# Performance work log

Measured on AMD Instinct MI355X. Metric: run time of the kernel, lower is better.

## Reference

```python
import jax, jax.numpy as jnp
import numpy as np

FS = 4096.0
TRAIN_KERNEL = 4
TRAIN_STRIDE = 0.25
BATCH = 1024
NPERSEG = 4096          # fftlength * fs
NOVERLAP = NPERSEG // 2 # default overlap
FL, FH = 20.0, 500.0


def _welch(data):
    """Faithful port of _torch_welch with average='mean' (which is a SUM over segments
    in the original code), off by the same constant factor as the original."""
    N, nsample = data.shape
    nstride = NPERSEG - NOVERLAP
    nseg = int(np.ceil((nsample - NPERSEG) / nstride)) + 1
    # frame indices [nseg, nperseg] (static numpy -> cheap gather)
    idx = np.arange(nseg)[:, None] * nstride + np.arange(NPERSEG)[None, :]
    frames = data[:, idx]                                   # [N, nseg, nperseg]
    n = np.arange(NPERSEG)
    window = (0.5 - 0.5 * np.cos(2.0 * np.pi * n / NPERSEG)).astype(np.float32) * 2.0  # periodic hann * 2
    fd = jnp.fft.rfft(frames * window, axis=-1)             # [N, nseg, nfreq]
    power = jnp.real(fd) ** 2 + jnp.imag(fd) ** 2
    psd = jnp.sum(power, axis=1)                            # original 'mean' branch uses sum
    T = nsample * FS
    return psd / T                                          # [N, nfreq]


def setup_inputs() -> dict:
    key = jax.random.key(0)
    k1, k2 = jax.random.split(key)
    T = int(TRAIN_KERNEL * FS)  # 16384
    pred = jax.random.normal(k1, (BATCH, T), dtype=jnp.float32)
    target = jax.random.normal(k2, (BATCH, T), dtype=jnp.float32)
    return {"pred": pred, "target": target}


def reference(pred, target):
    res = target - pred
    s = int(TRAIN_STRIDE * FS)                     # 1024 samples per stride
    shape_x = int(TRAIN_KERNEL / TRAIN_STRIDE)     # 16
    # cross[i] = res[:, i*s:(i+1)*s].flatten() -> reshape/transpose, no loop
    def to_cross(x):
        return x[:, : shape_x * s].reshape(BATCH, shape_x, s).transpose(1, 0, 2).reshape(shape_x, BATCH * s)
    cross_res = to_cross(res)
    cross_target = to_cross(target)

    psd_res = _welch(cross_res)                    # [shape_x, nfreq]
    psd_target = _welch(cross_target)

    nfreq = NPERSEG // 2 + 1
    freq = np.linspace(0.0, FS / 2.0, nfreq)
    mask = jnp.asarray((FL < freq) & (freq < FH))
    dfreq = float(freq[1] - freq[0])
    scale = FH - FL

    psd_res = jnp.where(mask, psd_res, 0.0)
    psd_ratio = psd_res / psd_target
    loss = jnp.sum(psd_ratio, axis=1) * dfreq / scale  # [shape_x]
    return jnp.mean(loss[-8:]) * loss.shape[0]
```

## Files before the change

### kernel.cpp

```cpp
#include <hip/hip_runtime.h>

#define NSEG 511
#define NROWS 8
#define ROW0 8
#define K0 21
#define KEND 500
#define NFREQ 479
#define ACC_STRIDE 512
#define ACC_ELEMS (2 * NROWS * ACC_STRIDE)
#define NREP 8
#define NBLOCKS (2 * NROWS * NSEG)

__device__ __forceinline__ int sw(int i) { return i ^ (((i >> 5) & 7) << 2); }

__device__ __forceinline__ int dr_pos(int k) {
    return ((k >> 9) & 3) + 4 * ((k >> 6) & 7) + 32 * ((k >> 3) & 7) + 256 * (k & 7);
}

__device__ __forceinline__ float2 cmul(float2 a, float2 b) {
    return make_float2(fmaf(a.x, b.x, -a.y * b.y), fmaf(a.x, b.y, a.y * b.x));
}
__device__ __forceinline__ float2 cadd(float2 a, float2 b) { return make_float2(a.x + b.x, a.y + b.y); }
__device__ __forceinline__ float2 csub(float2 a, float2 b) { return make_float2(a.x - b.x, a.y - b.y); }

__device__ __forceinline__ void dft8(float2& x0, float2& x1, float2& x2, float2& x3,
                                     float2& x4, float2& x5, float2& x6, float2& x7) {
    const float C45 = 0.70710678118654752440f;
    float2 t0 = cadd(x0, x4), u0 = csub(x0, x4);
    float2 t1 = cadd(x1, x5), u1 = csub(x1, x5);
    float2 t2 = cadd(x2, x6), u2 = csub(x2, x6);
    float2 t3 = cadd(x3, x7), u3 = csub(x3, x7);
    float2 s0 = cadd(t0, t2), d0 = csub(t0, t2);
    float2 s1 = cadd(t1, t3), d1 = csub(t1, t3);
    float2 v1 = make_float2(C45 * (u1.x + u1.y), C45 * (u1.y - u1.x));
    float2 v2 = make_float2(u2.y, -u2.x);
    float2 v3 = make_float2(C45 * (u3.y - u3.x), -C45 * (u3.x + u3.y));
    float2 s2 = cadd(u0, v2), d2 = csub(u0, v2);
    float2 s3 = cadd(v1, v3), d3 = csub(v1, v3);
    float2 mid1 = make_float2(d1.y, -d1.x);
    float2 mid3 = make_float2(d3.y, -d3.x);
    x0 = cadd(s0, s1); x4 = csub(s0, s1);
    x2 = cadd(d0, mid1); x6 = csub(d0, mid1);
    x1 = cadd(s2, s3); x5 = csub(s2, s3);
    x3 = cadd(d2, mid3); x7 = csub(d2, mid3);
}

__device__ __forceinline__ void twiddle8(float2& x1, float2& x2, float2& x3, float2& x4,
                                         float2& x5, float2& x6, float2& x7, float ang) {
    float s, c;
    __sincosf(ang, &s, &c);
    float2 w1 = make_float2(c, s);
    float2 w2 = cmul(w1, w1);
    float2 w3 = cmul(w2, w1);
    float2 w4 = cmul(w2, w2);
    float2 w5 = cmul(w4, w1);
    float2 w6 = cmul(w3, w3);
    float2 w7 = cmul(w4, w3);
    x1 = cmul(x1, w1); x2 = cmul(x2, w2); x3 = cmul(x3, w3);
    x4 = cmul(x4, w4); x5 = cmul(x5, w5); x6 = cmul(x6, w6);
    x7 = cmul(x7, w7);
}

__global__ __launch_bounds__(256)
void psd_kernel(const float* __restrict__ pred,
                const float* __restrict__ target,
                float* __restrict__ acc) {
    __shared__ float2 buf[2048];

    const int bid = blockIdx.x;
    const int seg = bid % NSEG;
    const int row = (bid / NSEG) % NROWS + ROW0;
    const int sig = bid / (NSEG * NROWS);
    const int tid = threadIdx.x;
    float* accR = acc + (bid & (NREP - 1)) * ACC_ELEMS;

    const float2* t2p = (const float2*)target;
    const float2* p2p = (const float2*)pred;

    const float WA = 3.06796157577128245e-3f;
    const float CD = 0.99999882344642529f;
    const float SD = 1.53398018628476550e-3f;
    const int base2 = 2 * seg * 8192 + row * 512 + tid;
    float2 x0, x1, x2, x3, x4, x5, x6, x7;
#define LOADW(R, X)                                                          \
    {                                                                        \
        int idx2 = base2 + ((R) >> 1) * 8192 + ((R) & 1) * 256;              \
        float2 v = t2p[idx2];                                                \
        if (sig == 0) { float2 p = p2p[idx2]; v.x -= p.x; v.y -= p.y; }      \
        float sa, ca;                                                        \
        __sincosf((float)(tid + 256 * (R)) * WA, &sa, &ca);                  \
        X = make_float2(v.x * (1.0f - ca),                                   \
                        v.y * (1.0f - (ca * CD - sa * SD)));                 \
    }
    LOADW(0, x0) LOADW(1, x1) LOADW(2, x2) LOADW(3, x3)
    LOADW(4, x4) LOADW(5, x5) LOADW(6, x6) LOADW(7, x7)
#undef LOADW

    dft8(x0, x1, x2, x3, x4, x5, x6, x7);
    twiddle8(x1, x2, x3, x4, x5, x6, x7, (float)tid * -3.06796157577128245e-3f);
    buf[sw(tid)]        = x0;
    buf[sw(tid + 256)]  = x1;
    buf[sw(tid + 512)]  = x2;
    buf[sw(tid + 768)]  = x3;
    buf[sw(tid + 1024)] = x4;
    buf[sw(tid + 1280)] = x5;
    buf[sw(tid + 1536)] = x6;
    buf[sw(tid + 1792)] = x7;
    __syncthreads();

    {
        const int pb = tid >> 5, q0 = tid & 31;
        const int baseB = q0 + 256 * pb;
        x0 = buf[sw(baseB)];
        x1 = buf[sw(baseB + 32)];
        x2 = buf[sw(baseB + 64)];
        x3 = buf[sw(baseB + 96)];
        x4 = buf[sw(baseB + 128)];
        x5 = buf[sw(baseB + 160)];
        x6 = buf[sw(baseB + 192)];
        x7 = buf[sw(baseB + 224)];
        dft8(x0, x1, x2, x3, x4, x5, x6, x7);
        twiddle8(x1, x2, x3, x4, x5, x6, x7, (float)q0 * -2.45436926061702596e-2f);
        buf[sw(baseB)]       = x0;
        buf[sw(baseB + 32)]  = x1;
        buf[sw(baseB + 64)]  = x2;
        buf[sw(baseB + 96)]  = x3;
        buf[sw(baseB + 128)] = x4;
        buf[sw(baseB + 160)] = x5;
        buf[sw(baseB + 192)] = x6;
        buf[sw(baseB + 224)] = x7;
    }
    __syncthreads();

    {
        const int pb2 = tid >> 5, j2 = (tid >> 2) & 7, mq = tid & 3;
        const int baseC = mq + 32 * j2 + 256 * pb2;
        x0 = buf[sw(baseC)];
        x1 = buf[sw(baseC + 4)];
        x2 = buf[sw(baseC + 8)];
        x3 = buf[sw(baseC + 12)];
        x4 = buf[sw(baseC + 16)];
        x5 = buf[sw(baseC + 20)];
        x6 = buf[sw(baseC + 24)];
        x7 = buf[sw(baseC + 28)];
        dft8(x0, x1, x2, x3, x4, x5, x6, x7);
        twiddle8(x1, x2, x3, x4, x5, x6, x7, (float)mq * -1.96349540849362077e-1f);
        buf[sw(baseC)]      = x0;
        buf[sw(baseC + 4)]  = x1;
        buf[sw(baseC + 8)]  = x2;
        buf[sw(baseC + 12)] = x3;
        buf[sw(baseC + 16)] = x4;
        buf[sw(baseC + 20)] = x5;
        buf[sw(baseC + 24)] = x6;
        buf[sw(baseC + 28)] = x7;
    }
    __syncthreads();

    float4* b4 = (float4*)buf;
#define STAGE_D(G)                                                           \
    {                                                                        \
        int pbase = sw(4 * (tid + 256 * (G)));                               \
        float4 lo = b4[(pbase >> 1)];                                        \
        float4 hi = b4[(pbase >> 1) + 1];                                    \
        float2 a0 = make_float2(lo.x, lo.y), a1 = make_float2(lo.z, lo.w);   \
        float2 a2 = make_float2(hi.x, hi.y), a3 = make_float2(hi.z, hi.w);   \
        float2 S0 = cadd(a0, a2), D0 = csub(a0, a2);                         \
        float2 S1 = cadd(a1, a3), D1 = csub(a1, a3);                         \
        float2 mi = make_float2(D1.y, -D1.x);                                \
        float2 X0 = cadd(S0, S1), X2 = csub(S0, S1);                         \
        float2 X1 = cadd(D0, mi), X3 = csub(D0, mi);                         \
        b4[(pbase >> 1)]     = make_float4(X0.x, X0.y, X1.x, X1.y);          \
        b4[(pbase >> 1) + 1] = make_float4(X2.x, X2.y, X3.x, X3.y);          \
    }
    STAGE_D(0) STAGE_D(1)
#undef STAGE_D
    __syncthreads();

#define UNTANGLE(RR)                                                         \
    {                                                                        \
        int k = K0 + tid + 256 * (RR);                                       \
        if (k < KEND) {                                                      \
            float2 zk = buf[sw(dr_pos(k))];                                  \
            float2 zn = buf[sw(dr_pos(2048 - k))];                           \
            float Ex = 0.5f * (zk.x + zn.x);                                 \
            float Ey = 0.5f * (zk.y - zn.y);                                 \
            float Ox = 0.5f * (zk.y + zn.y);                                 \
            float Oy = -0.5f * (zk.x - zn.x);                                \
            float sn, cs;                                                    \
            __sincosf(-1.53398078788564123e-3f * (float)k, &sn, &cs);        \
            float xr = Ex + Ox * cs - Oy * sn;                               \
            float xi = Ey + Ox * sn + Oy * cs;                               \
            float pw = xr * xr + xi * xi;                                    \
            atomicAdd(&accR[(sig * NROWS + (row - ROW0)) * ACC_STRIDE + (k - K0)], pw); \
        }                                                                    \
    }
    UNTANGLE(0) UNTANGLE(1)
#undef UNTANGLE
}

__global__ __launch_bounds__(256)
void reduce_kernel(const float* __restrict__ acc, float* __restrict__ out) {
    __shared__ float sh[256];
    int tid = threadIdx.x;
    float sum = 0.0f;
    for (int n = tid; n < NROWS * NFREQ; n += 256) {
        int r = n / NFREQ, k = n % NFREQ;
        float num = 0.0f, den = 0.0f;
        #pragma unroll
        for (int rep = 0; rep < NREP; ++rep) {
            num += acc[rep * ACC_ELEMS + r * ACC_STRIDE + k];
            den += acc[rep * ACC_ELEMS + (NROWS + r) * ACC_STRIDE + k];
        }
        sum += num / den;
    }
    sh[tid] = sum;
    __syncthreads();
    for (int s = 128; s > 0; s >>= 1) {
        if (tid < s) sh[tid] += sh[tid + s];
        __syncthreads();
    }
    if (tid == 0) out[0] = sh[0] * (1.0f / 240.0f);
}

extern "C" void kernel_launch(void* const* d_in, const int* in_sizes, int n_in,
                              void* d_out, int out_size, void* d_ws, size_t ws_size,
                              hipStream_t stream) {
    const float* pred = (const float*)d_in[0];
    const float* target = (const float*)d_in[1];
    float* acc = (float*)d_ws;

    hipMemsetAsync(acc, 0, NREP * ACC_ELEMS * sizeof(float), stream);
    psd_kernel<<<NBLOCKS, 256, 0, stream>>>(pred, target, acc);
    reduce_kernel<<<1, 256, 0, stream>>>(acc, (float*)d_out);
}
```

Before: 190.3 us.

## Fuse final radix-4 stage into untangle and cut sincos and barrier costs

The last radix-4 FFT stage is folded into the real-FFT untangle step. Each output bin now reads its four partial values straight from shared memory and combines them in registers, which removes one shared-memory pass and one block barrier. Per-element sincos calls are replaced with symmetry rotations of a single sincos, a small constant table and an incremental rotation for the second bin. One __syncthreads is swapped for an s_waitcnt, which is only safe because each wavefront writes and then reads only its own data. The k-to-thread mapping also changes, which alters the shared-memory access pattern and the atomic addresses, and rotation-based twiddles may differ slightly in precision.

```diff
diff --git a/kernel.cpp b/kernel.cpp
--- a/kernel.cpp
+++ b/kernel.cpp
@@ -12,10 +12,6 @@
 #define NBLOCKS (2 * NROWS * NSEG)
 
 __device__ __forceinline__ int sw(int i) { return i ^ (((i >> 5) & 7) << 2); }
-
-__device__ __forceinline__ int dr_pos(int k) {
-    return ((k >> 9) & 3) + 4 * ((k >> 6) & 7) + 32 * ((k >> 3) & 7) + 256 * (k & 7);
-}
 
 __device__ __forceinline__ float2 cmul(float2 a, float2 b) {
     return make_float2(fmaf(a.x, b.x, -a.y * b.y), fmaf(a.x, b.y, a.y * b.x));
@@ -45,10 +41,9 @@
     x3 = cadd(d2, mid3); x7 = csub(d2, mid3);
 }
 
-__device__ __forceinline__ void twiddle8(float2& x1, float2& x2, float2& x3, float2& x4,
-                                         float2& x5, float2& x6, float2& x7, float ang) {
-    float s, c;
-    __sincosf(ang, &s, &c);
+__device__ __forceinline__ void twiddle8cs(float2& x1, float2& x2, float2& x3, float2& x4,
+                                           float2& x5, float2& x6, float2& x7,
+                                           float c, float s) {
     float2 w1 = make_float2(c, s);
     float2 w2 = cmul(w1, w1);
     float2 w3 = cmul(w2, w1);
@@ -80,24 +75,33 @@
     const float WA = 3.06796157577128245e-3f;
     const float CD = 0.99999882344642529f;
     const float SD = 1.53398018628476550e-3f;
+    const float H  = 0.70710678118654752440f;
+    float sa, ca;
+    __sincosf((float)tid * WA, &sa, &ca);
+
     const int base2 = 2 * seg * 8192 + row * 512 + tid;
     float2 x0, x1, x2, x3, x4, x5, x6, x7;
-#define LOADW(R, X)                                                          \
+#define LOADW(R, X, CE, SE)                                                  \
     {                                                                        \
         int idx2 = base2 + ((R) >> 1) * 8192 + ((R) & 1) * 256;              \
         float2 v = t2p[idx2];                                                \
         if (sig == 0) { float2 p = p2p[idx2]; v.x -= p.x; v.y -= p.y; }      \
-        float sa, ca;                                                        \
-        __sincosf((float)(tid + 256 * (R)) * WA, &sa, &ca);                  \
-        X = make_float2(v.x * (1.0f - ca),                                   \
-                        v.y * (1.0f - (ca * CD - sa * SD)));                 \
-    }
-    LOADW(0, x0) LOADW(1, x1) LOADW(2, x2) LOADW(3, x3)
-    LOADW(4, x4) LOADW(5, x5) LOADW(6, x6) LOADW(7, x7)
+        float cr = (CE), sr = (SE);                                          \
+        X = make_float2(v.x * (1.0f - cr),                                   \
+                        v.y * (1.0f - (cr * CD - sr * SD)));                 \
+    }
+    LOADW(0, x0, ca, sa)
+    LOADW(1, x1, H * (ca - sa), H * (sa + ca))
+    LOADW(2, x2, -sa, ca)
+    LOADW(3, x3, -H * (ca + sa), H * (ca - sa))
+    LOADW(4, x4, -ca, -sa)
+    LOADW(5, x5, H * (sa - ca), -H * (sa + ca))
+    LOADW(6, x6, sa, -ca)
+    LOADW(7, x7, H * (ca + sa), H * (sa - ca))
 #undef LOADW
 
     dft8(x0, x1, x2, x3, x4, x5, x6, x7);
-    twiddle8(x1, x2, x3, x4, x5, x6, x7, (float)tid * -3.06796157577128245e-3f);
+    twiddle8cs(x1, x2, x3, x4, x5, x6, x7, ca, -sa);
     buf[sw(tid)]        = x0;
     buf[sw(tid + 256)]  = x1;
     buf[sw(tid + 512)]  = x2;
@@ -120,7 +124,9 @@
         x6 = buf[sw(baseB + 192)];
         x7 = buf[sw(baseB + 224)];
         dft8(x0, x1, x2, x3, x4, x5, x6, x7);
-        twiddle8(x1, x2, x3, x4, x5, x6, x7, (float)q0 * -2.45436926061702596e-2f);
+        float sb, cb;
+        __sincosf((float)q0 * -2.45436926061702596e-2f, &sb, &cb);
+        twiddle8cs(x1, x2, x3, x4, x5, x6, x7, cb, sb);
         buf[sw(baseB)]       = x0;
         buf[sw(baseB + 32)]  = x1;
         buf[sw(baseB + 64)]  = x2;
@@ -130,7 +136,7 @@
         buf[sw(baseB + 192)] = x6;
         buf[sw(baseB + 224)] = x7;
     }
-    __syncthreads();
+    asm volatile("s_waitcnt lgkmcnt(0)" ::: "memory");
 
     {
         const int pb2 = tid >> 5, j2 = (tid >> 2) & 7, mq = tid & 3;
@@ -144,7 +150,12 @@
         x6 = buf[sw(baseC + 24)];
         x7 = buf[sw(baseC + 28)];
         dft8(x0, x1, x2, x3, x4, x5, x6, x7);
-        twiddle8(x1, x2, x3, x4, x5, x6, x7, (float)mq * -1.96349540849362077e-1f);
+        const float TC1 = 0.98078528040323044913f, TS1 = -0.19509032201612826785f;
+        const float TC2 = 0.92387953251128675613f, TS2 = -0.38268343236508977173f;
+        const float TC3 = 0.83146961230254523708f, TS3 = -0.55557023301960222474f;
+        float cc = (mq & 2) ? ((mq & 1) ? TC3 : TC2) : ((mq & 1) ? TC1 : 1.0f);
+        float ss = (mq & 2) ? ((mq & 1) ? TS3 : TS2) : ((mq & 1) ? TS1 : 0.0f);
+        twiddle8cs(x1, x2, x3, x4, x5, x6, x7, cc, ss);
         buf[sw(baseC)]      = x0;
         buf[sw(baseC + 4)]  = x1;
         buf[sw(baseC + 8)]  = x2;
@@ -156,45 +167,44 @@
     }
     __syncthreads();
 
-    float4* b4 = (float4*)buf;
-#define STAGE_D(G)                                                           \
+    const int kk0 = K0 + (((tid & 7) << 6) | (tid >> 3));
+    float sn0, cs0;
+    __sincosf(-1.53398078788564123e-3f * (float)kk0, &sn0, &cs0);
+#define UNTANGLE(KK, CS, SN)                                                 \
     {                                                                        \
-        int pbase = sw(4 * (tid + 256 * (G)));                               \
-        float4 lo = b4[(pbase >> 1)];                                        \
-        float4 hi = b4[(pbase >> 1) + 1];                                    \
-        float2 a0 = make_float2(lo.x, lo.y), a1 = make_float2(lo.z, lo.w);   \
-        float2 a2 = make_float2(hi.x, hi.y), a3 = make_float2(hi.z, hi.w);   \
-        float2 S0 = cadd(a0, a2), D0 = csub(a0, a2);                         \
-        float2 S1 = cadd(a1, a3), D1 = csub(a1, a3);                         \
-        float2 mi = make_float2(D1.y, -D1.x);                                \
-        float2 X0 = cadd(S0, S1), X2 = csub(S0, S1);                         \
-        float2 X1 = cadd(D0, mi), X3 = csub(D0, mi);                         \
-        b4[(pbase >> 1)]     = make_float4(X0.x, X0.y, X1.x, X1.y);          \
-        b4[(pbase >> 1) + 1] = make_float4(X2.x, X2.y, X3.x, X3.y);          \
-    }
-    STAGE_D(0) STAGE_D(1)
-#undef STAGE_D
-    __syncthreads();
-
-#define UNTANGLE(RR)                                                         \
-    {                                                                        \
-        int k = K0 + tid + 256 * (RR);                                       \
-        if (k < KEND) {                                                      \
-            float2 zk = buf[sw(dr_pos(k))];                                  \
-            float2 zn = buf[sw(dr_pos(2048 - k))];                           \
+        int kk = (KK);                                                       \
+        if (kk < KEND) {                                                     \
+            int bk = 4 * ((kk >> 6) & 7) + 32 * ((kk >> 3) & 7) + 256 * (kk & 7); \
+            int sbk = sw(bk);                                                \
+            float2 a0 = buf[sbk], a1 = buf[sbk + 1];                         \
+            float2 a2 = buf[sbk + 2], a3 = buf[sbk + 3];                     \
+            float2 zk = make_float2((a0.x + a2.x) + (a1.x + a3.x),           \
+                                    (a0.y + a2.y) + (a1.y + a3.y));          \
+            int m = 2048 - kk;                                               \
+            int bm = 4 * ((m >> 6) & 7) + 32 * ((m >> 3) & 7) + 256 * (m & 7); \
+            int sbm = sw(bm);                                                \
+            float2 b0 = buf[sbm], b1 = buf[sbm + 1];                         \
+            float2 b2 = buf[sbm + 2], b3 = buf[sbm + 3];                     \
+            float2 zn = make_float2((b0.x - b2.x) - (b1.y - b3.y),           \
+                                    (b0.y - b2.y) + (b1.x - b3.x));          \
             float Ex = 0.5f * (zk.x + zn.x);                                 \
             float Ey = 0.5f * (zk.y - zn.y);                                 \
             float Ox = 0.5f * (zk.y + zn.y);                                 \
             float Oy = -0.5f * (zk.x - zn.x);                                \
-            float sn, cs;                                                    \
-            __sincosf(-1.53398078788564123e-3f * (float)k, &sn, &cs);        \
-            float xr = Ex + Ox * cs - Oy * sn;                               \
-            float xi = Ey + Ox * sn + Oy * cs;                               \
+            float xr = Ex + Ox * (CS) - Oy * (SN);                           \
+            float xi = Ey + Ox * (SN) + Oy * (CS);                           \
             float pw = xr * xr + xi * xi;                                    \
-            atomicAdd(&accR[(sig * NROWS + (row - ROW0)) * ACC_STRIDE + (k - K0)], pw); \
+            atomicAdd(&accR[(sig * NROWS + (row - ROW0)) * ACC_STRIDE + (kk - K0)], pw); \
         }                                                                    \
     }
-    UNTANGLE(0) UNTANGLE(1)
+    UNTANGLE(kk0, cs0, sn0)
+    {
+        const float CU = 0.99879545620517240501f;
+        const float SU = 0.04906767432741801426f;
+        float cs1 = cs0 * CU + sn0 * SU;
+        float sn1 = sn0 * CU - cs0 * SU;
+        UNTANGLE(kk0 + 32, cs1, sn1)
+    }
 #undef UNTANGLE
 }
 
```

Result: slower. 224.8 us (+18.1%).
